# Optimization experiments

Hardware: AMD Instinct MI355X
Metric: run time of the kernel (lower is better)

The kernel has to match this reference:

```python
import jax, jax.numpy as jnp
import numpy as np

GR = 16

def _conv(x, w, b, pad):
    y = jax.lax.conv_general_dilated(x, w, (1, 1), [(pad, pad), (pad, pad)],
                                     dimension_numbers=('NCHW', 'OIHW', 'NCHW'))
    return y + b[None, :, None, None]

def _build_stencil(h, w):
    num = h * w
    a = np.zeros((num, 4, num), np.float32)
    i = np.arange(num)
    m0 = ((i + 1) % w != 0) & (i + 1 < num)
    a[i[m0], 0, i[m0]] = 1.0; a[i[m0], 0, i[m0] + 1] = -1.0
    m1 = i + w < num
    a[i[m1], 1, i[m1]] = 1.0; a[i[m1], 1, i[m1] + w] = -1.0
    m2 = ((i + 2) % w != 0) & (i + 2 < num)
    a[i[m2], 2, i[m2]] = 1.0; a[i[m2], 2, i[m2] + 2] = -1.0
    m3 = i + 2 * w < num
    a[i[m3], 3, i[m3]] = 1.0; a[i[m3], 3, i[m3] + 2 * w] = -1.0
    a[-1, 0, -1] = 1.0; a[-1, 1, -1] = 1.0; a[-1, 2, -1] = 1.0; a[-1, 3, -1] = 1.0
    return jnp.asarray(a)  # (num, 4, num)

def setup_inputs() -> dict:
    key = jax.random.key(0)
    ks = jax.random.split(key, 20)
    n, c, h, w = 4, 64, 24, 24
    s = 0.02
    inp = {
        'x': jax.random.normal(ks[0], (n, c, h, w), jnp.float32),
        'a': _build_stencil(h, w),
        'grad_w1': jax.random.normal(ks[1], (c, c, 3, 3)) * s,
        'grad_b1': jnp.zeros((c,)),
        'grad_w2': jax.random.normal(ks[2], (4 * GR, c, 3, 3)) * s,
        'grad_b2': jnp.zeros((4 * GR,)),
        'att_w1': jax.random.normal(ks[3], (c, c, 3, 3)) * s,
        'att_b1': jnp.zeros((c,)),
        'att_w2': jax.random.normal(ks[4], (4 * GR, c, 3, 3)) * s,
        'att_b2': jnp.zeros((4 * GR,)),
        'se_w1': jax.random.normal(ks[5], (c // 2, c, 1, 1)) * s,
        'se_b1': jnp.zeros((c // 2,)),
        'se_w2': jax.random.normal(ks[6], (GR, c // 2, 1, 1)) * s,
        'se_b2': jnp.zeros((GR,)),
        'gn_w': jnp.ones((GR,)),
        'gn_b': jnp.zeros((GR,)),
        'post_w': jax.random.normal(ks[7], (8 * GR, GR, 3, 3)) * s,
        'post_b': jnp.zeros((8 * GR,)),
    }
    return inp

def reference(x, a, grad_w1, grad_b1, grad_w2, grad_b2,
              att_w1, att_b1, att_w2, att_b2,
              se_w1, se_b1, se_w2, se_b2,
              gn_w, gn_b, post_w, post_b):
    n, c, h, w = x.shape
    num = h * w
    # attention branch: conv -> leaky_relu -> conv -> sigmoid
    att = jax.nn.sigmoid(_conv(jax.nn.leaky_relu(_conv(x, att_w1, att_b1, 1), 0.01), att_w2, att_b2, 1))
    # gradient branch: conv -> leaky_relu -> conv
    grad = _conv(jax.nn.leaky_relu(_conv(x, grad_w1, grad_b1, 1), 0.01), grad_w2, grad_b2, 1)
    # squeeze-excite: GAP -> 1x1 conv -> leaky -> 1x1 conv -> sigmoid
    pooled = x.mean(axis=(2, 3), keepdims=True)  # (n,c,1,1)
    se = jax.nn.sigmoid(_conv(jax.nn.leaky_relu(_conv(pooled, se_w1, se_b1, 0), 0.01), se_w2, se_b2, 0))
    # reshape per-pixel 4-tap weights: (n*GR, num, 4, 1)
    att_r = att.reshape(n * GR, 4, num, 1).transpose(0, 2, 1, 3)
    grad_r = grad.reshape(n * GR, 4, num, 1).transpose(0, 2, 1, 3)
    # densified weighted stencil operator
    A = a[None] * att_r                      # (b, num, 4, num)
    B = (grad_r * att_r)[..., 0]             # (b, num, 4)
    A = A.reshape(n * GR, num * 4, num)      # (b, 4num, num)
    B = B.reshape(n * GR, num * 4)           # (b, 4num)
    ATA = jnp.einsum('bkn,bkm->bnm', A, A)   # (b, num, num)
    ATB = jnp.einsum('bkn,bk->bn', A, B)[..., None]
    ATA = ATA + jnp.eye(num, dtype=x.dtype)[None] * 1e-12
    sol = jnp.linalg.solve(ATA, ATB)         # (b, num, 1)
    y = sol.reshape(n, GR, h, w)
    # GroupNorm(1, GR): normalize over all channels + spatial, eps=1e-5
    mu = y.mean(axis=(1, 2, 3), keepdims=True)
    var = y.var(axis=(1, 2, 3), keepdims=True)
    y = (y - mu) / jnp.sqrt(var + 1e-5)
    y = y * gn_w[None, :, None, None] + gn_b[None, :, None, None]
    y = se * y
    return _conv(y, post_w, post_b, 1)
```

## Files before the change

### kernel.cpp

```cpp
#include <hip/hip_runtime.h>
#include <math.h>

#define NUM 576
#define BSTR 50
#define CTH 512
#define CHOL_LDS_BYTES ((NUM * BSTR + CTH) * sizeof(float))

__device__ __forceinline__ float leakyf(float v) { return v > 0.f ? v : 0.01f * v; }
__device__ __forceinline__ float sigmoidf(float v) { return 1.f / (1.f + __expf(-v)); }
__device__ __forceinline__ float rdlane(float v, int l) {
  return __uint_as_float(__builtin_amdgcn_readlane(__float_as_uint(v), l));
}

__global__ __launch_bounds__(576) void conv1se_kernel(
    const float* __restrict__ x,
    const float* __restrict__ wa, const float* __restrict__ ba,
    const float* __restrict__ wg, const float* __restrict__ bg,
    const float* __restrict__ sw1, const float* __restrict__ sb1,
    const float* __restrict__ sw2, const float* __restrict__ sb2,
    float* __restrict__ outa, float* __restrict__ outg,
    float* __restrict__ sev, double* __restrict__ acc)
{
  __shared__ float sx[16 * 576];
  __shared__ float pooled[64];
  __shared__ float hid[32];
  const int co = blockIdx.x, n = blockIdx.y;
  const int tid = threadIdx.x;

  if (co == 64) {
    if (tid < 2) acc[n * 2 + tid] = 0.0;
    if (tid < 64) {
      const float4* xp4 = (const float4*)(x + (size_t)(n * 64 + tid) * 576);
      float s = 0.f;
      for (int p = 0; p < 144; ++p) {
        float4 v = xp4[p];
        s += v.x + v.y + v.z + v.w;
      }
      pooled[tid] = s * (1.f / 576.f);
    }
    __syncthreads();
    if (tid < 32) {
      float h = sb1[tid];
      for (int c = 0; c < 64; ++c) h += pooled[c] * sw1[tid * 64 + c];
      hid[tid] = leakyf(h);
    }
    __syncthreads();
    if (tid < 16) {
      float v = sb2[tid];
      for (int j = 0; j < 32; ++j) v += hid[j] * sw2[tid * 32 + j];
      sev[n * 16 + tid] = sigmoidf(v);
    }
    return;
  }

  const int py = tid / 24, px = tid - py * 24;
  float acc_a = ba[co];
  float acc_g = bg[co];
  for (int c0 = 0; c0 < 64; c0 += 16) {
    __syncthreads();
    {
      const float4* xs4 = (const float4*)(x + (size_t)(n * 64 + c0) * 576);
      float4* sx4 = (float4*)sx;
#pragma unroll
      for (int q = 0; q < 4; ++q) sx4[tid + q * 576] = xs4[tid + q * 576];
    }
    __syncthreads();
#pragma unroll 4
    for (int k = 0; k < 16; ++k) {
      const float* wpa = wa + (co * 64 + c0 + k) * 9;
      const float* wpg = wg + (co * 64 + c0 + k) * 9;
#pragma unroll
      for (int dy = 0; dy < 3; ++dy) {
        const int yy = py + dy - 1;
        const bool oky = (unsigned)yy < 24u;
        const int iy = yy < 0 ? 0 : (yy > 23 ? 23 : yy);
#pragma unroll
        for (int dx = 0; dx < 3; ++dx) {
          const int xx = px + dx - 1;
          const bool ok = oky && ((unsigned)xx < 24u);
          const int ix = xx < 0 ? 0 : (xx > 23 ? 23 : xx);
          const float v = ok ? sx[k * 576 + iy * 24 + ix] : 0.f;
          acc_a += v * wpa[dy * 3 + dx];
          acc_g += v * wpg[dy * 3 + dx];
        }
      }
    }
  }
  const int o = (n * 64 + co) * 576 + tid;
  outa[o] = leakyf(acc_a);
  outg[o] = leakyf(acc_g);
}

__global__ __launch_bounds__(576) void conv2_kernel(
    const float* __restrict__ t1a, const float* __restrict__ t1g,
    const float* __restrict__ wa, const float* __restrict__ ba,
    const float* __restrict__ wg, const float* __restrict__ bg,
    float* __restrict__ att, float* __restrict__ grd)
{
  __shared__ float sx[16 * 576];
  const int co = blockIdx.x, n = blockIdx.y, br = blockIdx.z;
  const float* src = br ? t1g : t1a;
  const float* wp0 = br ? wg : wa;
  const float bias = br ? bg[co] : ba[co];
  float* dst = br ? grd : att;
  const int tid = threadIdx.x;
  const int py = tid / 24, px = tid - py * 24;
  float acc = bias;
  for (int c0 = 0; c0 < 64; c0 += 16) {
    __syncthreads();
    {
      const float4* s4 = (const float4*)(src + (size_t)(n * 64 + c0) * 576);
      float4* sx4 = (float4*)sx;
#pragma unroll
      for (int q = 0; q < 4; ++q) sx4[tid + q * 576] = s4[tid + q * 576];
    }
    __syncthreads();
#pragma unroll 4
    for (int k = 0; k < 16; ++k) {
      const float* wp = wp0 + (co * 64 + c0 + k) * 9;
#pragma unroll
      for (int dy = 0; dy < 3; ++dy) {
        const int yy = py + dy - 1;
        const bool oky = (unsigned)yy < 24u;
        const int iy = yy < 0 ? 0 : (yy > 23 ? 23 : yy);
#pragma unroll
        for (int dx = 0; dx < 3; ++dx) {
          const int xx = px + dx - 1;
          const bool ok = oky && ((unsigned)xx < 24u);
          const int ix = xx < 0 ? 0 : (xx > 23 ? 23 : xx);
          const float v = ok ? sx[k * 576 + iy * 24 + ix] : 0.f;
          acc += v * wp[dy * 3 + dx];
        }
      }
    }
  }
  if (br == 0) acc = sigmoidf(acc);
  dst[(n * 64 + co) * 576 + tid] = acc;
}

__global__ __launch_bounds__(CTH, 1) void chol_kernel(
    const float* __restrict__ att, const float* __restrict__ grd,
    float* __restrict__ sol, double* __restrict__ acc)
{
  extern __shared__ float S[];
  __shared__ float RHS_s[NUM];
  __shared__ float RD_s[NUM];
  __shared__ float XS_s[NUM];
  __shared__ __align__(16) float CP[8][64];
  __shared__ float DUMW[64];
  __shared__ double RW[16];
  const int b = blockIdx.x, tid = threadIdx.x;
  const int n = b >> 4, g = b & 15;
  const float* ac = att + (size_t)(n * 64 + g * 4) * 576;
  const float* gc = grd + (size_t)(n * 64 + g * 4) * 576;

  int r1A, r2A;
  {
    const int T = (tid < 300) ? tid : 0;
    int U = (int)((sqrtf(8.f * (float)T + 1.f) - 1.f) * 0.5f);
    while (U * (U + 1) / 2 > T) --U;
    while ((U + 1) * (U + 2) / 2 <= T) ++U;
    const int W = T - U * (U + 1) / 2;
    r1A = (tid < 300) ? (8 + 2 * U) : 63;
    r2A = 8 + 2 * W;
  }

  for (int i = tid; i < NUM * BSTR; i += CTH) S[i] = 0.f;
  __syncthreads();

  for (int i = tid; i < NUM; i += CTH) {
    float diag = 1e-12f, rv = 0.f;
    float od1 = 0.f, od2 = 0.f, od24 = 0.f, od48 = 0.f;
    if (((i + 1) % 24 != 0) && (i + 1 < NUM)) {
      float a0 = ac[0 * 576 + i]; float s = a0 * a0;
      diag += s; rv += s * gc[0 * 576 + i];
    }
    if (i - 1 >= 0 && (i % 24 != 0)) {
      float a0 = ac[0 * 576 + (i - 1)]; float s = a0 * a0;
      diag += s; rv -= s * gc[0 * 576 + (i - 1)]; od1 = -s;
    }
    if (i + 24 < NUM) {
      float a1 = ac[1 * 576 + i]; float s = a1 * a1;
      diag += s; rv += s * gc[1 * 576 + i];
    }
    if (i - 24 >= 0) {
      float a1 = ac[1 * 576 + (i - 24)]; float s = a1 * a1;
      diag += s; rv -= s * gc[1 * 576 + (i - 24)]; od24 = -s;
    }
    if (((i + 2) % 24 != 0) && (i + 2 < NUM)) {
      float a2 = ac[2 * 576 + i]; float s = a2 * a2;
      diag += s; rv += s * gc[2 * 576 + i];
    }
    if (i - 2 >= 0 && (i % 24 != 0)) {
      float a2 = ac[2 * 576 + (i - 2)]; float s = a2 * a2;
      diag += s; rv -= s * gc[2 * 576 + (i - 2)]; od2 = -s;
    }
    if (i + 48 < NUM) {
      float a3 = ac[3 * 576 + i]; float s = a3 * a3;
      diag += s; rv += s * gc[3 * 576 + i];
    }
    if (i - 48 >= 0) {
      float a3 = ac[3 * 576 + (i - 48)]; float s = a3 * a3;
      diag += s; rv -= s * gc[3 * 576 + (i - 48)]; od48 = -s;
    }
    if (i == NUM - 1) {
#pragma unroll
      for (int t = 0; t < 4; ++t) {
        float a = ac[t * 576 + (NUM - 1)]; float s = a * a;
        diag += s; rv += s * gc[t * 576 + (NUM - 1)];
      }
    }
    S[i * BSTR + 0] = diag;
    S[i * BSTR + 1] = od1;
    S[i * BSTR + 2] = od2;
    S[i * BSTR + 24] = od24;
    S[i * BSTR + 48] = od48;
    RHS_s[i] = rv;
    if (i == 0) RD_s[0] = rsqrtf(diag);
  }

  for (int j = 0; j < NUM; j += 8) {
    __syncthreads();
    if (tid < 64) {
      const int t = tid;
      const int row = j + t;
      const bool rok = row < NUM;
      float v[8];
#pragma unroll
      for (int c = 0; c < 8; ++c) {
        const bool okc = rok && (t >= c) && (t - c <= 48);
        const int addr = okc ? (row * BSTR + (t - c)) : (NUM * BSTR + t);
        float vv = S[addr];
        v[c] = okc ? vv : 0.f;
      }
      float zb[8];
#pragma unroll
      for (int k = 0; k < 8; ++k) zb[k] = RHS_s[j + k];
      float z = RHS_s[rok ? row : j];
      z = rok ? z : 0.f;
      const float rd0 = RD_s[j];
      float rdv[8], y[8], lp[8][8];
#pragma unroll
      for (int k = 0; k < 8; ++k) {
        if (k == 0) {
          rdv[0] = rd0;
        } else {
          const float dk = rdlane(v[k], k);
          rdv[k] = rsqrtf(dk);
        }
        v[k] *= rdv[k];
#pragma unroll
        for (int m = k + 1; m < 8; ++m) {
          lp[m][k] = rdlane(v[k], m);
          v[m] -= v[k] * lp[m][k];
        }
      }
      y[0] = zb[0] * rdv[0];
#pragma unroll
      for (int k = 1; k < 8; ++k) {
        float a = zb[k];
#pragma unroll
        for (int m = 0; m < 8; ++m)
          if (m < k) a -= lp[k][m] * y[m];
        y[k] = a * rdv[k];
      }
      float zn = z;
#pragma unroll
      for (int c = 0; c < 8; ++c) zn -= v[c] * y[c];
#pragma unroll
      for (int c = 0; c < 8; ++c) {
        const bool okc = rok && (t > c) && (t - c <= 48);
        float* bp = okc ? &S[row * BSTR + (t - c)] : &S[NUM * BSTR + t];
        *bp = v[c];
        CP[c][t] = okc ? v[c] : 0.f;
      }
      if (t < 8) {
        float yv = y[0], rv = rdv[0];
#pragma unroll
        for (int k = 1; k < 8; ++k) {
          yv = (t == k) ? y[k] : yv;
          rv = (t == k) ? rdv[k] : rv;
        }
        RHS_s[row] = yv;
        RD_s[row] = rv;
      } else {
        float* rp = rok ? &RHS_s[row] : &DUMW[t & 63];
        *rp = zn;
      }
    }
    __syncthreads();
    const int R = (NUM - 1) - j;
    {
      const bool a0 = (r1A <= R);
      const bool a1 = (r1A + 1 <= R);
      float2 cr[8], cc[8];
#pragma unroll
      for (int c = 0; c < 8; ++c) {
        cr[c] = *(const float2*)&CP[c][r1A & 62];
        cc[c] = *(const float2*)&CP[c][r2A];
      }
      float s00 = 0.f, s01 = 0.f, s10 = 0.f, s11 = 0.f;
#pragma unroll
      for (int c = 0; c < 8; ++c) {
        s00 += cr[c].x * cc[c].x; s01 += cr[c].x * cc[c].y;
        s10 += cr[c].y * cc[c].x; s11 += cr[c].y * cc[c].y;
      }
      const int p00 = j * BSTR + 51 * r1A - r2A;
      float* q00 = a0 ? &S[p00] : &S[NUM * BSTR + tid];
      float* q01 = a0 ? &S[p00 - 1] : &S[NUM * BSTR + tid];
      float* q10 = a1 ? &S[p00 + 51] : &S[NUM * BSTR + tid];
      float* q11 = a1 ? &S[p00 + 50] : &S[NUM * BSTR + tid];
      const float t00 = *q00 - s00, t01 = *q01 - s01;
      const float t10 = *q10 - s10, t11 = *q11 - s11;
      *q00 = t00; *q01 = t01; *q10 = t10; *q11 = t11;
      if (tid == 0 && a0)
        RD_s[j + 8] = rsqrtf(t00);
    }
  }
  __syncthreads();

  if (tid < 64) {
    const int t = tid;
    for (int i = NUM - 1; i >= 7; i -= 8) {
      asm volatile("s_waitcnt lgkmcnt(0)" ::: "memory");
      float zz[8], rr[8];
#pragma unroll
      for (int k = 0; k < 8; ++k) { zz[k] = RHS_s[i - k]; rr[k] = RD_s[i - k]; }
      float L[8][8];
#pragma unroll
      for (int a = 0; a < 8; ++a)
#pragma unroll
        for (int bb = 0; bb < 8; ++bb)
          if (bb > a) L[a][bb] = S[(i - a) * BSTR + (bb - a)];
      float x[8];
      x[0] = zz[0] * rr[0];
#pragma unroll
      for (int k = 1; k < 8; ++k) {
        float a = zz[k];
#pragma unroll
        for (int m = 0; m < 8; ++m)
          if (m < k) a -= L[m][k] * x[m];
        x[k] = a * rr[k];
      }
      const int rb = i - 8 - t;
      const bool bok = rb >= 0;
      float acc2 = 0.f;
#pragma unroll
      for (int k = 0; k < 8; ++k) {
        const int d = 8 + t - k;
        const bool ok = bok && (d <= 48);
        float Lv = S[ok ? ((i - k) * BSTR + d) : (NUM * BSTR + t)];
        Lv = ok ? Lv : 0.f;
        acc2 += Lv * x[k];
      }
      const float zbv = RHS_s[bok ? rb : 0];
      float* rp = bok ? &RHS_s[rb] : &DUMW[t];
      *rp = zbv - acc2;
      float xv = x[0];
#pragma unroll
      for (int k = 1; k < 8; ++k) xv = (t == k) ? x[k] : xv;
      if (t < 8) XS_s[i - t] = xv;
    }
  }
  __syncthreads();

  double ls = 0.0, ls2 = 0.0;
  for (int i = tid; i < NUM; i += CTH) {
    const float xv = XS_s[i];
    sol[(size_t)b * NUM + i] = xv;
    ls += (double)xv;
    ls2 += (double)xv * (double)xv;
  }
#pragma unroll
  for (int off = 32; off > 0; off >>= 1) {
    ls += __shfl_down(ls, off);
    ls2 += __shfl_down(ls2, off);
  }
  if ((tid & 63) == 0) {
    RW[(tid >> 6) * 2] = ls;
    RW[(tid >> 6) * 2 + 1] = ls2;
  }
  __syncthreads();
  if (tid == 0) {
    double s = 0.0, s2 = 0.0;
#pragma unroll
    for (int wv = 0; wv < 8; ++wv) { s += RW[wv * 2]; s2 += RW[wv * 2 + 1]; }
    atomicAdd(&acc[n * 2], s);
    atomicAdd(&acc[n * 2 + 1], s2);
  }
}

__global__ __launch_bounds__(576) void postgn_kernel(
    const float* __restrict__ sol, const double* __restrict__ acc,
    const float* __restrict__ sev,
    const float* __restrict__ gnw, const float* __restrict__ gnb,
    const float* __restrict__ w, const float* __restrict__ bias,
    float* __restrict__ out)
{
  __shared__ float sy[16 * 576];
  const int co = blockIdx.x, n = blockIdx.y, tid = threadIdx.x;
  const double mu_d = acc[n * 2] * (1.0 / 9216.0);
  const double var_d = acc[n * 2 + 1] * (1.0 / 9216.0) - mu_d * mu_d;
  const float rstd = (float)(1.0 / sqrt(var_d + 1e-5));
  const float muf = (float)mu_d;
  {
    const float4* sp4 = (const float4*)(sol + (size_t)n * 9216);
    float4* sy4 = (float4*)sy;
#pragma unroll
    for (int q = 0; q < 4; ++q) {
      const int p = tid + q * 576;
      const int k = p / 144;
      const float sv = sev[n * 16 + k];
      const float A = rstd * gnw[k] * sv;
      const float B = (gnb[k] - muf * rstd * gnw[k]) * sv;
      float4 v = sp4[p];
      v.x = v.x * A + B; v.y = v.y * A + B;
      v.z = v.z * A + B; v.w = v.w * A + B;
      sy4[p] = v;
    }
  }
  __syncthreads();
  const int py = tid / 24, px = tid - py * 24;
  float a = bias[co];
#pragma unroll 4
  for (int k = 0; k < 16; ++k) {
    const float* wp = w + (co * 16 + k) * 9;
#pragma unroll
    for (int dy = 0; dy < 3; ++dy) {
      const int yy = py + dy - 1;
      const bool oky = (unsigned)yy < 24u;
      const int iy = yy < 0 ? 0 : (yy > 23 ? 23 : yy);
#pragma unroll
      for (int dx = 0; dx < 3; ++dx) {
        const int xx = px + dx - 1;
        const bool ok = oky && ((unsigned)xx < 24u);
        const int ix = xx < 0 ? 0 : (xx > 23 ? 23 : xx);
        const float v = ok ? sy[k * 576 + iy * 24 + ix] : 0.f;
        a += v * wp[dy * 3 + dx];
      }
    }
  }
  out[(size_t)(n * 128 + co) * 576 + tid] = a;
}

extern "C" void kernel_launch(void* const* d_in, const int* in_sizes, int n_in,
                              void* d_out, int out_size, void* d_ws, size_t ws_size,
                              hipStream_t stream) {
  const float* x       = (const float*)d_in[0];
  const float* grad_w1 = (const float*)d_in[2];
  const float* grad_b1 = (const float*)d_in[3];
  const float* grad_w2 = (const float*)d_in[4];
  const float* grad_b2 = (const float*)d_in[5];
  const float* att_w1  = (const float*)d_in[6];
  const float* att_b1  = (const float*)d_in[7];
  const float* att_w2  = (const float*)d_in[8];
  const float* att_b2  = (const float*)d_in[9];
  const float* se_w1   = (const float*)d_in[10];
  const float* se_b1   = (const float*)d_in[11];
  const float* se_w2   = (const float*)d_in[12];
  const float* se_b2   = (const float*)d_in[13];
  const float* gn_w    = (const float*)d_in[14];
  const float* gn_b    = (const float*)d_in[15];
  const float* post_w  = (const float*)d_in[16];
  const float* post_b  = (const float*)d_in[17];
  float* out = (float*)d_out;

  float* ws  = (float*)d_ws;
  float* t1a = ws;
  float* t1g = t1a + 147456;
  float* att = t1g + 147456;
  float* grd = att + 147456;
  float* sev = grd + 147456;
  float* sol = sev + 64;
  double* acc = (double*)(sol + 36864);

  (void)hipFuncSetAttribute((const void*)chol_kernel,
                            hipFuncAttributeMaxDynamicSharedMemorySize,
                            (int)CHOL_LDS_BYTES);

  conv1se_kernel<<<dim3(65, 4), 576, 0, stream>>>(
      x, att_w1, att_b1, grad_w1, grad_b1,
      se_w1, se_b1, se_w2, se_b2, t1a, t1g, sev, acc);
  conv2_kernel<<<dim3(64, 4, 2), 576, 0, stream>>>(t1a, t1g, att_w2, att_b2,
                                                   grad_w2, grad_b2, att, grd);
  chol_kernel<<<64, CTH, CHOL_LDS_BYTES, stream>>>(att, grd, sol, acc);
  postgn_kernel<<<dim3(128, 4), 576, 0, stream>>>(sol, acc, sev, gn_w, gn_b,
                                                  post_w, post_b, out);
}
```

Measured before the change: 198.8 us.

## Two-sided banded Cholesky factorization and zero-padded halo conv tiles

The banded Cholesky solve now factors from both ends of the matrix at once. One wavefront eliminates forward from the top, a second eliminates in reversed order from the bottom, and the two fronts meet in a middle block. This roughly halves the number of sequential panel steps on the serial critical path, at the cost of a more complicated coupling step and back-substitution. Separately, all three convolution kernels now stage inputs into zero-padded 26x26 LDS tiles, removing per-tap bounds checks and clamping at the cost of extra LDS and scattered scalar stores.

```diff
diff --git a/kernel.cpp b/kernel.cpp
--- a/kernel.cpp
+++ b/kernel.cpp
@@ -21,7 +21,7 @@
     float* __restrict__ outa, float* __restrict__ outg,
     float* __restrict__ sev, double* __restrict__ acc)
 {
-  __shared__ float sx[16 * 576];
+  __shared__ float sx[16 * 676];
   __shared__ float pooled[64];
   __shared__ float hid[32];
   const int co = blockIdx.x, n = blockIdx.y;
@@ -54,36 +54,37 @@
   }
 
   const int py = tid / 24, px = tid - py * 24;
+  const int hb0 = py * 26 + px;
+  for (int i = tid; i < 16 * 676; i += 576) sx[i] = 0.f;
   float acc_a = ba[co];
   float acc_g = bg[co];
   for (int c0 = 0; c0 < 64; c0 += 16) {
     __syncthreads();
-    {
-      const float4* xs4 = (const float4*)(x + (size_t)(n * 64 + c0) * 576);
-      float4* sx4 = (float4*)sx;
-#pragma unroll
-      for (int q = 0; q < 4; ++q) sx4[tid + q * 576] = xs4[tid + q * 576];
+#pragma unroll
+    for (int q = 0; q < 4; ++q) {
+      const int p = tid + q * 576;
+      const int k = p / 144;
+      const int r = p - k * 144;
+      const int pix = r * 4;
+      const int ppy = pix / 24, ppx = pix - ppy * 24;
+      const float4 v = *(const float4*)&x[(size_t)(n * 64 + c0) * 576 + p * 4];
+      float* d = &sx[k * 676 + (ppy + 1) * 26 + ppx + 1];
+      d[0] = v.x; d[1] = v.y; d[2] = v.z; d[3] = v.w;
     }
     __syncthreads();
 #pragma unroll 4
     for (int k = 0; k < 16; ++k) {
       const float* wpa = wa + (co * 64 + c0 + k) * 9;
       const float* wpg = wg + (co * 64 + c0 + k) * 9;
-#pragma unroll
-      for (int dy = 0; dy < 3; ++dy) {
-        const int yy = py + dy - 1;
-        const bool oky = (unsigned)yy < 24u;
-        const int iy = yy < 0 ? 0 : (yy > 23 ? 23 : yy);
+      const float* sp = &sx[k * 676 + hb0];
+#pragma unroll
+      for (int dy = 0; dy < 3; ++dy)
 #pragma unroll
         for (int dx = 0; dx < 3; ++dx) {
-          const int xx = px + dx - 1;
-          const bool ok = oky && ((unsigned)xx < 24u);
-          const int ix = xx < 0 ? 0 : (xx > 23 ? 23 : xx);
-          const float v = ok ? sx[k * 576 + iy * 24 + ix] : 0.f;
+          const float v = sp[dy * 26 + dx];
           acc_a += v * wpa[dy * 3 + dx];
           acc_g += v * wpg[dy * 3 + dx];
         }
-      }
     }
   }
   const int o = (n * 64 + co) * 576 + tid;
@@ -97,7 +98,7 @@
     const float* __restrict__ wg, const float* __restrict__ bg,
     float* __restrict__ att, float* __restrict__ grd)
 {
-  __shared__ float sx[16 * 576];
+  __shared__ float sx[16 * 676];
   const int co = blockIdx.x, n = blockIdx.y, br = blockIdx.z;
   const float* src = br ? t1g : t1a;
   const float* wp0 = br ? wg : wa;
@@ -105,37 +106,166 @@
   float* dst = br ? grd : att;
   const int tid = threadIdx.x;
   const int py = tid / 24, px = tid - py * 24;
+  const int hb0 = py * 26 + px;
+  for (int i = tid; i < 16 * 676; i += 576) sx[i] = 0.f;
   float acc = bias;
   for (int c0 = 0; c0 < 64; c0 += 16) {
     __syncthreads();
-    {
-      const float4* s4 = (const float4*)(src + (size_t)(n * 64 + c0) * 576);
-      float4* sx4 = (float4*)sx;
-#pragma unroll
-      for (int q = 0; q < 4; ++q) sx4[tid + q * 576] = s4[tid + q * 576];
+#pragma unroll
+    for (int q = 0; q < 4; ++q) {
+      const int p = tid + q * 576;
+      const int k = p / 144;
+      const int r = p - k * 144;
+      const int pix = r * 4;
+      const int ppy = pix / 24, ppx = pix - ppy * 24;
+      const float4 v = *(const float4*)&src[(size_t)(n * 64 + c0) * 576 + p * 4];
+      float* d = &sx[k * 676 + (ppy + 1) * 26 + ppx + 1];
+      d[0] = v.x; d[1] = v.y; d[2] = v.z; d[3] = v.w;
     }
     __syncthreads();
 #pragma unroll 4
     for (int k = 0; k < 16; ++k) {
       const float* wp = wp0 + (co * 64 + c0 + k) * 9;
-#pragma unroll
-      for (int dy = 0; dy < 3; ++dy) {
-        const int yy = py + dy - 1;
-        const bool oky = (unsigned)yy < 24u;
-        const int iy = yy < 0 ? 0 : (yy > 23 ? 23 : yy);
-#pragma unroll
-        for (int dx = 0; dx < 3; ++dx) {
-          const int xx = px + dx - 1;
-          const bool ok = oky && ((unsigned)xx < 24u);
-          const int ix = xx < 0 ? 0 : (xx > 23 ? 23 : xx);
-          const float v = ok ? sx[k * 576 + iy * 24 + ix] : 0.f;
-          acc += v * wp[dy * 3 + dx];
-        }
-      }
+      const float* sp = &sx[k * 676 + hb0];
+#pragma unroll
+      for (int dy = 0; dy < 3; ++dy)
+#pragma unroll
+        for (int dx = 0; dx < 3; ++dx)
+          acc += sp[dy * 26 + dx] * wp[dy * 3 + dx];
     }
   }
   if (br == 0) acc = sigmoidf(acc);
   dst[(n * 64 + co) * 576 + tid] = acc;
+}
+
+__device__ __forceinline__ void scale_panel_f(
+    float* __restrict__ S, float* RHS_s, float* RD_s, float (*CP)[64],
+    float* DUMW, int t, int j, int maxrow, int dumidx)
+{
+  const int row = j + t;
+  const bool rok = row <= maxrow;
+  float v[8];
+#pragma unroll
+  for (int c = 0; c < 8; ++c) {
+    const bool okc = rok && (t >= c) && (t - c <= 48);
+    const int addr = okc ? (row * BSTR + (t - c)) : dumidx;
+    float vv = S[addr];
+    v[c] = okc ? vv : 0.f;
+  }
+  float zb[8];
+#pragma unroll
+  for (int k = 0; k < 8; ++k) zb[k] = RHS_s[j + k];
+  float z = RHS_s[rok ? row : j];
+  z = rok ? z : 0.f;
+  float rdv[8], y[8], lp[8][8];
+#pragma unroll
+  for (int k = 0; k < 8; ++k) {
+    if (k == 0) rdv[0] = RD_s[j];
+    else rdv[k] = rsqrtf(rdlane(v[k], k));
+    v[k] *= rdv[k];
+#pragma unroll
+    for (int m = k + 1; m < 8; ++m) {
+      lp[m][k] = rdlane(v[k], m);
+      v[m] -= v[k] * lp[m][k];
+    }
+  }
+  y[0] = zb[0] * rdv[0];
+#pragma unroll
+  for (int k = 1; k < 8; ++k) {
+    float a = zb[k];
+#pragma unroll
+    for (int m = 0; m < 8; ++m)
+      if (m < k) a -= lp[k][m] * y[m];
+    y[k] = a * rdv[k];
+  }
+  float zn = z;
+#pragma unroll
+  for (int c = 0; c < 8; ++c) zn -= v[c] * y[c];
+#pragma unroll
+  for (int c = 0; c < 8; ++c) {
+    const bool okc = rok && (t > c) && (t - c <= 48);
+    float* bp = okc ? &S[row * BSTR + (t - c)] : &S[dumidx];
+    *bp = v[c];
+    CP[c][t] = okc ? v[c] : 0.f;
+  }
+  if (t < 8) {
+    float yv = y[0], rv = rdv[0];
+#pragma unroll
+    for (int k = 1; k < 8; ++k) {
+      yv = (t == k) ? y[k] : yv;
+      rv = (t == k) ? rdv[k] : rv;
+    }
+    RHS_s[row] = yv;
+    RD_s[row] = rv;
+  } else {
+    float* rp = rok ? &RHS_s[row] : &DUMW[t & 63];
+    *rp = zn;
+  }
+}
+
+__device__ __forceinline__ void scale_panel_b(
+    float* __restrict__ S, float* RHS_s, float* RD_s, float (*CP)[64],
+    float* DUMW, int t, int jf, int dumidx)
+{
+  const int rr = jf + t;
+  const bool rok = rr <= 287;
+  float v[8];
+#pragma unroll
+  for (int c = 0; c < 8; ++c) {
+    const bool okc = rok && (t >= c) && (t - c <= 48);
+    const int addr = okc ? ((575 - rr + (t - c)) * BSTR + (t - c)) : dumidx;
+    float vv = S[addr];
+    v[c] = okc ? vv : 0.f;
+  }
+  float zb[8];
+#pragma unroll
+  for (int k = 0; k < 8; ++k) zb[k] = RHS_s[575 - (jf + k)];
+  float z = RHS_s[rok ? (575 - rr) : (575 - jf)];
+  z = rok ? z : 0.f;
+  float rdv[8], y[8], lp[8][8];
+#pragma unroll
+  for (int k = 0; k < 8; ++k) {
+    if (k == 0) rdv[0] = RD_s[575 - jf];
+    else rdv[k] = rsqrtf(rdlane(v[k], k));
+    v[k] *= rdv[k];
+#pragma unroll
+    for (int m = k + 1; m < 8; ++m) {
+      lp[m][k] = rdlane(v[k], m);
+      v[m] -= v[k] * lp[m][k];
+    }
+  }
+  y[0] = zb[0] * rdv[0];
+#pragma unroll
+  for (int k = 1; k < 8; ++k) {
+    float a = zb[k];
+#pragma unroll
+    for (int m = 0; m < 8; ++m)
+      if (m < k) a -= lp[k][m] * y[m];
+    y[k] = a * rdv[k];
+  }
+  float zn = z;
+#pragma unroll
+  for (int c = 0; c < 8; ++c) zn -= v[c] * y[c];
+#pragma unroll
+  for (int c = 0; c < 8; ++c) {
+    const bool okc = rok && (t > c) && (t - c <= 48);
+    float* bp = okc ? &S[(575 - rr + (t - c)) * BSTR + (t - c)] : &S[dumidx];
+    *bp = v[c];
+    CP[c][t] = okc ? v[c] : 0.f;
+  }
+  if (t < 8) {
+    float yv = y[0], rv = rdv[0];
+#pragma unroll
+    for (int k = 1; k < 8; ++k) {
+      yv = (t == k) ? y[k] : yv;
+      rv = (t == k) ? rdv[k] : rv;
+    }
+    RHS_s[575 - rr] = yv;
+    RD_s[575 - rr] = rv;
+  } else {
+    float* rp = rok ? &RHS_s[575 - rr] : &DUMW[t & 63];
+    *rp = zn;
+  }
 }
 
 __global__ __launch_bounds__(CTH, 1) void chol_kernel(
@@ -146,23 +276,33 @@
   __shared__ float RHS_s[NUM];
   __shared__ float RD_s[NUM];
   __shared__ float XS_s[NUM];
-  __shared__ __align__(16) float CP[8][64];
+  __shared__ __align__(16) float CPF[8][64];
+  __shared__ __align__(16) float CPB[8][64];
   __shared__ float DUMW[64];
   __shared__ double RW[16];
   const int b = blockIdx.x, tid = threadIdx.x;
   const int n = b >> 4, g = b & 15;
   const float* ac = att + (size_t)(n * 64 + g * 4) * 576;
   const float* gc = grd + (size_t)(n * 64 + g * 4) * 576;
-
-  int r1A, r2A;
+  const int dumidx = NUM * BSTR + tid;
+
+  int r1A, r2A, r1B, r2B;
+  const bool okA = tid < 300;
+  const int btid = (tid >= 300) ? (tid - 300) : ((tid < 88) ? (tid + 212) : -1);
+  const bool okB = btid >= 0;
   {
-    const int T = (tid < 300) ? tid : 0;
+    int T = okA ? tid : 0;
     int U = (int)((sqrtf(8.f * (float)T + 1.f) - 1.f) * 0.5f);
     while (U * (U + 1) / 2 > T) --U;
     while ((U + 1) * (U + 2) / 2 <= T) ++U;
-    const int W = T - U * (U + 1) / 2;
-    r1A = (tid < 300) ? (8 + 2 * U) : 63;
-    r2A = 8 + 2 * W;
+    int W = T - U * (U + 1) / 2;
+    r1A = 8 + 2 * U; r2A = 8 + 2 * W;
+    T = okB ? btid : 0;
+    U = (int)((sqrtf(8.f * (float)T + 1.f) - 1.f) * 0.5f);
+    while (U * (U + 1) / 2 > T) --U;
+    while ((U + 1) * (U + 2) / 2 <= T) ++U;
+    W = T - U * (U + 1) / 2;
+    r1B = 8 + 2 * U; r2B = 8 + 2 * W;
   }
 
   for (int i = tid; i < NUM * BSTR; i += CTH) S[i] = 0.f;
@@ -217,87 +357,23 @@
     S[i * BSTR + 48] = od48;
     RHS_s[i] = rv;
     if (i == 0) RD_s[0] = rsqrtf(diag);
-  }
-
-  for (int j = 0; j < NUM; j += 8) {
-    __syncthreads();
-    if (tid < 64) {
-      const int t = tid;
-      const int row = j + t;
-      const bool rok = row < NUM;
-      float v[8];
+    if (i == NUM - 1) RD_s[NUM - 1] = rsqrtf(diag);
+  }
+
+  for (int s = 0; s < 30; ++s) {
+    const int j = 8 * s;
+    __syncthreads();
+    if (tid < 64)
+      scale_panel_f(S, RHS_s, RD_s, CPF, DUMW, tid, j, 287, dumidx);
+    else if (tid < 128)
+      scale_panel_b(S, RHS_s, RD_s, CPB, DUMW, tid - 64, j, dumidx);
+    __syncthreads();
+    {
+      float2 cr[8], cc[8];
 #pragma unroll
       for (int c = 0; c < 8; ++c) {
-        const bool okc = rok && (t >= c) && (t - c <= 48);
-        const int addr = okc ? (row * BSTR + (t - c)) : (NUM * BSTR + t);
-        float vv = S[addr];
-        v[c] = okc ? vv : 0.f;
-      }
-      float zb[8];
-#pragma unroll
-      for (int k = 0; k < 8; ++k) zb[k] = RHS_s[j + k];
-      float z = RHS_s[rok ? row : j];
-      z = rok ? z : 0.f;
-      const float rd0 = RD_s[j];
-      float rdv[8], y[8], lp[8][8];
-#pragma unroll
-      for (int k = 0; k < 8; ++k) {
-        if (k == 0) {
-          rdv[0] = rd0;
-        } else {
-          const float dk = rdlane(v[k], k);
-          rdv[k] = rsqrtf(dk);
-        }
-        v[k] *= rdv[k];
-#pragma unroll
-        for (int m = k + 1; m < 8; ++m) {
-          lp[m][k] = rdlane(v[k], m);
-          v[m] -= v[k] * lp[m][k];
-        }
-      }
-      y[0] = zb[0] * rdv[0];
-#pragma unroll
-      for (int k = 1; k < 8; ++k) {
-        float a = zb[k];
-#pragma unroll
-        for (int m = 0; m < 8; ++m)
-          if (m < k) a -= lp[k][m] * y[m];
-        y[k] = a * rdv[k];
-      }
-      float zn = z;
-#pragma unroll
-      for (int c = 0; c < 8; ++c) zn -= v[c] * y[c];
-#pragma unroll
-      for (int c = 0; c < 8; ++c) {
-        const bool okc = rok && (t > c) && (t - c <= 48);
-        float* bp = okc ? &S[row * BSTR + (t - c)] : &S[NUM * BSTR + t];
-        *bp = v[c];
-        CP[c][t] = okc ? v[c] : 0.f;
-      }
-      if (t < 8) {
-        float yv = y[0], rv = rdv[0];
-#pragma unroll
-        for (int k = 1; k < 8; ++k) {
-          yv = (t == k) ? y[k] : yv;
-          rv = (t == k) ? rdv[k] : rv;
-        }
-        RHS_s[row] = yv;
-        RD_s[row] = rv;
-      } else {
-        float* rp = rok ? &RHS_s[row] : &DUMW[t & 63];
-        *rp = zn;
-      }
-    }
-    __syncthreads();
-    const int R = (NUM - 1) - j;
-    {
-      const bool a0 = (r1A <= R);
-      const bool a1 = (r1A + 1 <= R);
-      float2 cr[8], cc[8];
-#pragma unroll
-      for (int c = 0; c < 8; ++c) {
-        cr[c] = *(const float2*)&CP[c][r1A & 62];
-        cc[c] = *(const float2*)&CP[c][r2A];
+        cr[c] = *(const float2*)&CPF[c][r1A];
+        cc[c] = *(const float2*)&CPF[c][r2A];
       }
       float s00 = 0.f, s01 = 0.f, s10 = 0.f, s11 = 0.f;
 #pragma unroll
@@ -306,26 +382,81 @@
         s10 += cr[c].y * cc[c].x; s11 += cr[c].y * cc[c].y;
       }
       const int p00 = j * BSTR + 51 * r1A - r2A;
-      float* q00 = a0 ? &S[p00] : &S[NUM * BSTR + tid];
-      float* q01 = a0 ? &S[p00 - 1] : &S[NUM * BSTR + tid];
-      float* q10 = a1 ? &S[p00 + 51] : &S[NUM * BSTR + tid];
-      float* q11 = a1 ? &S[p00 + 50] : &S[NUM * BSTR + tid];
+      float* q00 = okA ? &S[p00] : &S[dumidx];
+      float* q01 = okA ? &S[p00 - 1] : &S[dumidx];
+      float* q10 = okA ? &S[p00 + 51] : &S[dumidx];
+      float* q11 = okA ? &S[p00 + 50] : &S[dumidx];
       const float t00 = *q00 - s00, t01 = *q01 - s01;
       const float t10 = *q10 - s10, t11 = *q11 - s11;
       *q00 = t00; *q01 = t01; *q10 = t10; *q11 = t11;
-      if (tid == 0 && a0)
-        RD_s[j + 8] = rsqrtf(t00);
+      if (tid == 0) RD_s[j + 8] = rsqrtf(t00);
+    }
+    {
+      float2 cr[8], cc[8];
+#pragma unroll
+      for (int c = 0; c < 8; ++c) {
+        cr[c] = *(const float2*)&CPB[c][r1B];
+        cc[c] = *(const float2*)&CPB[c][r2B];
+      }
+      float s00 = 0.f, s01 = 0.f, s10 = 0.f, s11 = 0.f;
+#pragma unroll
+      for (int c = 0; c < 8; ++c) {
+        s00 += cr[c].x * cc[c].x; s01 += cr[c].x * cc[c].y;
+        s10 += cr[c].y * cc[c].x; s11 += cr[c].y * cc[c].y;
+      }
+      const int p00b = (575 - j - r2B) * BSTR + (r1B - r2B);
+      float* q00 = okB ? &S[p00b] : &S[dumidx];
+      float* q01 = okB ? &S[p00b - 51] : &S[dumidx];
+      float* q10 = okB ? &S[p00b + 1] : &S[dumidx];
+      float* q11 = okB ? &S[p00b - 50] : &S[dumidx];
+      const float t00 = *q00 - s00, t01 = *q01 - s01;
+      const float t10 = *q10 - s10, t11 = *q11 - s11;
+      *q00 = t00; *q01 = t01; *q10 = t10; *q11 = t11;
+      if (btid == 0 && j + 8 <= 239) RD_s[575 - (j + 8)] = rsqrtf(t00);
+    }
+  }
+
+  for (int j = 240; j < 336; j += 8) {
+    __syncthreads();
+    if (tid < 64)
+      scale_panel_f(S, RHS_s, RD_s, CPF, DUMW, tid, j, 335, dumidx);
+    __syncthreads();
+    const int R = 335 - j;
+    {
+      const bool a0 = okA && (r1A <= R);
+      const bool a1 = okA && (r1A + 1 <= R);
+      float2 cr[8], cc[8];
+#pragma unroll
+      for (int c = 0; c < 8; ++c) {
+        cr[c] = *(const float2*)&CPF[c][r1A];
+        cc[c] = *(const float2*)&CPF[c][r2A];
+      }
+      float s00 = 0.f, s01 = 0.f, s10 = 0.f, s11 = 0.f;
+#pragma unroll
+      for (int c = 0; c < 8; ++c) {
+        s00 += cr[c].x * cc[c].x; s01 += cr[c].x * cc[c].y;
+        s10 += cr[c].y * cc[c].x; s11 += cr[c].y * cc[c].y;
+      }
+      const int p00 = j * BSTR + 51 * r1A - r2A;
+      float* q00 = a0 ? &S[p00] : &S[dumidx];
+      float* q01 = a0 ? &S[p00 - 1] : &S[dumidx];
+      float* q10 = a1 ? &S[p00 + 51] : &S[dumidx];
+      float* q11 = a1 ? &S[p00 + 50] : &S[dumidx];
+      const float t00 = *q00 - s00, t01 = *q01 - s01;
+      const float t10 = *q10 - s10, t11 = *q11 - s11;
+      *q00 = t00; *q01 = t01; *q10 = t10; *q11 = t11;
+      if (tid == 0 && a0) RD_s[j + 8] = rsqrtf(t00);
     }
   }
   __syncthreads();
 
   if (tid < 64) {
     const int t = tid;
-    for (int i = NUM - 1; i >= 7; i -= 8) {
+    for (int i = 335; i >= 247; i -= 8) {
       asm volatile("s_waitcnt lgkmcnt(0)" ::: "memory");
-      float zz[8], rr[8];
-#pragma unroll
-      for (int k = 0; k < 8; ++k) { zz[k] = RHS_s[i - k]; rr[k] = RD_s[i - k]; }
+      float zz[8], rr2[8];
+#pragma unroll
+      for (int k = 0; k < 8; ++k) { zz[k] = RHS_s[i - k]; rr2[k] = RD_s[i - k]; }
       float L[8][8];
 #pragma unroll
       for (int a = 0; a < 8; ++a)
@@ -333,14 +464,14 @@
         for (int bb = 0; bb < 8; ++bb)
           if (bb > a) L[a][bb] = S[(i - a) * BSTR + (bb - a)];
       float x[8];
-      x[0] = zz[0] * rr[0];
+      x[0] = zz[0] * rr2[0];
 #pragma unroll
       for (int k = 1; k < 8; ++k) {
-        float a = zz[k];
+        float a2 = zz[k];
 #pragma unroll
         for (int m = 0; m < 8; ++m)
-          if (m < k) a -= L[m][k] * x[m];
-        x[k] = a * rr[k];
+          if (m < k) a2 -= L[m][k] * x[m];
+        x[k] = a2 * rr2[k];
       }
       const int rb = i - 8 - t;
       const bool bok = rb >= 0;
@@ -349,7 +480,7 @@
       for (int k = 0; k < 8; ++k) {
         const int d = 8 + t - k;
         const bool ok = bok && (d <= 48);
-        float Lv = S[ok ? ((i - k) * BSTR + d) : (NUM * BSTR + t)];
+        float Lv = S[ok ? ((i - k) * BSTR + d) : dumidx];
         Lv = ok ? Lv : 0.f;
         acc2 += Lv * x[k];
       }
@@ -360,6 +491,105 @@
 #pragma unroll
       for (int k = 1; k < 8; ++k) xv = (t == k) ? x[k] : xv;
       if (t < 8) XS_s[i - t] = xv;
+    }
+  }
+  __syncthreads();
+
+  if (tid < 48) {
+    const int jj = 336 + tid;
+    float sacc = 0.f;
+    for (int i = jj - 48; i <= 335; ++i)
+      sacc += S[jj * BSTR + (jj - i)] * XS_s[i];
+    RHS_s[jj] -= sacc;
+  }
+  __syncthreads();
+
+  if (tid < 64) {
+    const int t = tid;
+    for (int i = 239; i >= 7; i -= 8) {
+      asm volatile("s_waitcnt lgkmcnt(0)" ::: "memory");
+      float zz[8], rr2[8];
+#pragma unroll
+      for (int k = 0; k < 8; ++k) { zz[k] = RHS_s[i - k]; rr2[k] = RD_s[i - k]; }
+      float L[8][8];
+#pragma unroll
+      for (int a = 0; a < 8; ++a)
+#pragma unroll
+        for (int bb = 0; bb < 8; ++bb)
+          if (bb > a) L[a][bb] = S[(i - a) * BSTR + (bb - a)];
+      float x[8];
+      x[0] = zz[0] * rr2[0];
+#pragma unroll
+      for (int k = 1; k < 8; ++k) {
+        float a2 = zz[k];
+#pragma unroll
+        for (int m = 0; m < 8; ++m)
+          if (m < k) a2 -= L[m][k] * x[m];
+        x[k] = a2 * rr2[k];
+      }
+      const int rb = i - 8 - t;
+      const bool bok = rb >= 0;
+      float acc2 = 0.f;
+#pragma unroll
+      for (int k = 0; k < 8; ++k) {
+        const int d = 8 + t - k;
+        const bool ok = bok && (d <= 48);
+        float Lv = S[ok ? ((i - k) * BSTR + d) : dumidx];
+        Lv = ok ? Lv : 0.f;
+        acc2 += Lv * x[k];
+      }
+      const float zbv = RHS_s[bok ? rb : 0];
+      float* rp = bok ? &RHS_s[rb] : &DUMW[t];
+      *rp = zbv - acc2;
+      float xv = x[0];
+#pragma unroll
+      for (int k = 1; k < 8; ++k) xv = (t == k) ? x[k] : xv;
+      if (t < 8) XS_s[i - t] = xv;
+    }
+  } else if (tid < 128) {
+    const int t = tid - 64;
+    for (int i = 239; i >= 7; i -= 8) {
+      asm volatile("s_waitcnt lgkmcnt(0)" ::: "memory");
+      float zz[8], rr2[8];
+#pragma unroll
+      for (int k = 0; k < 8; ++k) {
+        zz[k] = RHS_s[575 - (i - k)];
+        rr2[k] = RD_s[575 - (i - k)];
+      }
+      float L[8][8];
+#pragma unroll
+      for (int a = 0; a < 8; ++a)
+#pragma unroll
+        for (int bb = 0; bb < 8; ++bb)
+          if (bb > a) L[a][bb] = S[(575 - (i - bb)) * BSTR + (bb - a)];
+      float x[8];
+      x[0] = zz[0] * rr2[0];
+#pragma unroll
+      for (int k = 1; k < 8; ++k) {
+        float a2 = zz[k];
+#pragma unroll
+        for (int m = 0; m < 8; ++m)
+          if (m < k) a2 -= L[m][k] * x[m];
+        x[k] = a2 * rr2[k];
+      }
+      const int rb = i - 8 - t;
+      const bool bok = rb >= 0;
+      float acc2 = 0.f;
+#pragma unroll
+      for (int k = 0; k < 8; ++k) {
+        const int d = 8 + t - k;
+        const bool ok = bok && (d <= 48);
+        float Lv = S[ok ? ((575 - rb) * BSTR + d) : dumidx];
+        Lv = ok ? Lv : 0.f;
+        acc2 += Lv * x[k];
+      }
+      const float zbv = RHS_s[bok ? (575 - rb) : 575];
+      float* rp = bok ? &RHS_s[575 - rb] : &DUMW[t];
+      *rp = zbv - acc2;
+      float xv = x[0];
+#pragma unroll
+      for (int k = 1; k < 8; ++k) xv = (t == k) ? x[k] : xv;
+      if (t < 8) XS_s[575 - (i - t)] = xv;
     }
   }
   __syncthreads();
@@ -397,48 +627,43 @@
     const float* __restrict__ w, const float* __restrict__ bias,
     float* __restrict__ out)
 {
-  __shared__ float sy[16 * 576];
+  __shared__ float sy[16 * 676];
   const int co = blockIdx.x, n = blockIdx.y, tid = threadIdx.x;
   const double mu_d = acc[n * 2] * (1.0 / 9216.0);
   const double var_d = acc[n * 2 + 1] * (1.0 / 9216.0) - mu_d * mu_d;
   const float rstd = (float)(1.0 / sqrt(var_d + 1e-5));
   const float muf = (float)mu_d;
-  {
-    const float4* sp4 = (const float4*)(sol + (size_t)n * 9216);
-    float4* sy4 = (float4*)sy;
-#pragma unroll
-    for (int q = 0; q < 4; ++q) {
-      const int p = tid + q * 576;
-      const int k = p / 144;
-      const float sv = sev[n * 16 + k];
-      const float A = rstd * gnw[k] * sv;
-      const float B = (gnb[k] - muf * rstd * gnw[k]) * sv;
-      float4 v = sp4[p];
-      v.x = v.x * A + B; v.y = v.y * A + B;
-      v.z = v.z * A + B; v.w = v.w * A + B;
-      sy4[p] = v;
-    }
+  for (int i = tid; i < 16 * 676; i += 576) sy[i] = 0.f;
+  __syncthreads();
+#pragma unroll
+  for (int q = 0; q < 4; ++q) {
+    const int p = tid + q * 576;
+    const int k = p / 144;
+    const int r = p - k * 144;
+    const int pix = r * 4;
+    const int ppy = pix / 24, ppx = pix - ppy * 24;
+    const float sv = sev[n * 16 + k];
+    const float gw = gnw[k] * rstd;
+    const float A = gw * sv;
+    const float B = (gnb[k] - muf * gw) * sv;
+    const float4 v = *(const float4*)&sol[(size_t)n * 9216 + p * 4];
+    float* d = &sy[k * 676 + (ppy + 1) * 26 + ppx + 1];
+    d[0] = v.x * A + B; d[1] = v.y * A + B;
+    d[2] = v.z * A + B; d[3] = v.w * A + B;
   }
   __syncthreads();
   const int py = tid / 24, px = tid - py * 24;
+  const int hb0 = py * 26 + px;
   float a = bias[co];
 #pragma unroll 4
   for (int k = 0; k < 16; ++k) {
     const float* wp = w + (co * 16 + k) * 9;
-#pragma unroll
-    for (int dy = 0; dy < 3; ++dy) {
-      const int yy = py + dy - 1;
-      const bool oky = (unsigned)yy < 24u;
-      const int iy = yy < 0 ? 0 : (yy > 23 ? 23 : yy);
-#pragma unroll
-      for (int dx = 0; dx < 3; ++dx) {
-        const int xx = px + dx - 1;
-        const bool ok = oky && ((unsigned)xx < 24u);
-        const int ix = xx < 0 ? 0 : (xx > 23 ? 23 : xx);
-        const float v = ok ? sy[k * 576 + iy * 24 + ix] : 0.f;
-        a += v * wp[dy * 3 + dx];
-      }
-    }
+    const float* sp = &sy[k * 676 + hb0];
+#pragma unroll
+    for (int dy = 0; dy < 3; ++dy)
+#pragma unroll
+      for (int dx = 0; dx < 3; ++dx)
+        a += sp[dy * 26 + dx] * wp[dy * 3 + dx];
   }
   out[(size_t)(n * 128 + co) * 576 + tid] = a;
 }
```

New measurement: 172.0 us. -13.5%, faster.
